# Kernel tuning notes

Hardware: AMD Instinct MI355X
Metric: run time of the kernel (lower is better)

## Reference

```python
import jax, jax.numpy as jnp
import numpy as np

# Dimensions (babyGPT-50m: GPT-2-small-ish)
B, T, V, C, H, L = 2, 1024, 50257, 768, 12, 6
D = C // H
STD = 0.02
EPS = 1e-5


def _normal(k, shape):
    return (jax.random.normal(k, shape, dtype=jnp.float32) * STD)


def setup_inputs() -> dict:
    key = jax.random.key(0)
    ks = jax.random.split(key, 12)
    inp = {
        "idx": jax.random.randint(ks[0], (B, T), 0, V, dtype=jnp.int64 if jax.config.jax_enable_x64 else jnp.int32),
        "tok_emb": _normal(ks[1], (V, C)),
        "pos_emb": _normal(ks[2], (1, T, C)),
        # per-layer params stacked along leading L axis
        "ln1_g": jnp.ones((L, C), jnp.float32),
        "ln1_b": jnp.zeros((L, C), jnp.float32),
        "Wq": _normal(ks[3], (L, C, C)), "bq": jnp.zeros((L, C), jnp.float32),
        "Wk": _normal(ks[4], (L, C, C)), "bk": jnp.zeros((L, C), jnp.float32),
        "Wv": _normal(ks[5], (L, C, C)), "bv": jnp.zeros((L, C), jnp.float32),
        "Wp": _normal(ks[6], (L, C, C)), "bp": jnp.zeros((L, C), jnp.float32),
        "ln2_g": jnp.ones((L, C), jnp.float32),
        "ln2_b": jnp.zeros((L, C), jnp.float32),
        "Wf1": _normal(ks[7], (L, C, 4 * C)), "bf1": jnp.zeros((L, 4 * C), jnp.float32),
        "Wf2": _normal(ks[8], (L, 4 * C, C)), "bf2": jnp.zeros((L, C), jnp.float32),
        "lnf_g": jnp.ones((C,), jnp.float32),
        "lnf_b": jnp.zeros((C,), jnp.float32),
        "head_W": _normal(ks[9], (C, V)),  # head has bias=False
    }
    return inp


def _ln(x, g, b):
    m = jnp.mean(x, axis=-1, keepdims=True)
    v = jnp.var(x, axis=-1, keepdims=True)
    return (x - m) * jax.lax.rsqrt(v + EPS) * g + b


def _gpt_forward(idx, tok_emb, pos_emb, ln1_g, ln1_b, Wq, bq, Wk, bk, Wv, bv,
                 Wp, bp, ln2_g, ln2_b, Wf1, bf1, Wf2, bf2, lnf_g, lnf_b, head_W):
    x = tok_emb[idx] + pos_emb[:, :T]          # [B,T,C]; dropout is identity (eval)
    causal = jnp.tril(jnp.ones((T, T), bool))  # same tril mask as the buffer
    scale = 1.0 / np.sqrt(D).astype(np.float32)

    def block(x, p):
        g1, b1, wq, bq_, wk, bk_, wv, bv_, wp, bp_, g2, b2, w1, b1f, w2, b2f = p
        h = _ln(x, g1, b1)
        q = (h @ wq + bq_).reshape(B, T, H, D)
        k = (h @ wk + bk_).reshape(B, T, H, D)
        v = (h @ wv + bv_).reshape(B, T, H, D)
        att = jnp.einsum('bthd,bshd->bhts', q, k) * scale   # [B,H,T,T]
        att = jnp.where(causal, att, jnp.float32(-10000.0))  # masked_fill value
        att = jax.nn.softmax(att, axis=-1)
        y = jnp.einsum('bhts,bshd->bthd', att, v).reshape(B, T, C)
        x = x + y @ wp + bp_
        h2 = _ln(x, g2, b2)
        ff = jax.nn.gelu(h2 @ w1 + b1f, approximate=False) @ w2 + b2f  # exact GELU, dropout=eval
        return x + ff, None

    layer_params = (ln1_g, ln1_b, Wq, bq, Wk, bk, Wv, bv, Wp, bp,
                    ln2_g, ln2_b, Wf1, bf1, Wf2, bf2)
    x, _ = jax.lax.scan(block, x, layer_params)
    x = _ln(x, lnf_g, lnf_b)
    return x @ head_W  # logits [B,T,V]


def reference(idx, tok_emb, pos_emb, ln1_g, ln1_b, Wq, bq, Wk, bk, Wv, bv,
              Wp, bp, ln2_g, ln2_b, Wf1, bf1, Wf2, bf2, lnf_g, lnf_b, head_W):
    return _gpt_forward(idx, tok_emb, pos_emb, ln1_g, ln1_b, Wq, bq, Wk, bk, Wv, bv,
                        Wp, bp, ln2_g, ln2_b, Wf1, bf1, Wf2, bf2, lnf_g, lnf_b, head_W)
```

## Files before the change

### kernel.cpp

```cpp
#include <hip/hip_runtime.h>
#include <hip/hip_bf16.h>
#include <math.h>

#define Bsz 2
#define Tt 1024
#define Vv 50257
#define Cc 768
#define Hh 12
#define Ll 6
#define NTOK (Bsz*Tt)
#define VPAD 50432

typedef __attribute__((ext_vector_type(8))) short bf16x8;
typedef __attribute__((ext_vector_type(8))) unsigned short u16x8;
typedef __attribute__((ext_vector_type(4))) unsigned short u16x4;
typedef __attribute__((ext_vector_type(4))) float f32x4;
typedef unsigned short u16;

static __device__ __forceinline__ u16 f2bf(float f){
  unsigned u = __float_as_uint(f);
  u += 0x7FFF + ((u >> 16) & 1);
  return (u16)(u >> 16);
}
static __device__ __forceinline__ float bf2f(u16 h){
  return __uint_as_float(((unsigned)h) << 16);
}

#define GL16(g,l) __builtin_amdgcn_global_load_lds( \
    (const __attribute__((address_space(1))) void*)(g), \
    (__attribute__((address_space(3))) void*)(l), 16, 0, 0)
#define WAITVM(n) asm volatile("s_waitcnt vmcnt(%0)" :: "n"(n) : "memory")

__global__ void embed_kernel(const int* __restrict__ idx, const float* __restrict__ tok,
                             const float* __restrict__ pos, float* __restrict__ x){
  const int C4 = Cc/4;
  int i = blockIdx.x * 256 + threadIdx.x;
  if (i >= NTOK*C4) return;
  int tk = i / C4, c4 = i % C4;
  int row = idx[tk];
  int t = tk % Tt;
  float4 a = ((const float4*)tok)[(size_t)row*C4 + c4];
  float4 p = ((const float4*)pos)[(size_t)t*C4 + c4];
  float4 r; r.x=a.x+p.x; r.y=a.y+p.y; r.z=a.z+p.z; r.w=a.w+p.w;
  ((float4*)x)[i] = r;
}

__global__ void ln_kernel(const float* __restrict__ in, const float* __restrict__ g,
                          const float* __restrict__ bt, u16* __restrict__ out){
  int row = blockIdx.x, tid = threadIdx.x;
  const float* r = in + (size_t)row*Cc;
  float v0=r[tid], v1=r[tid+256], v2=r[tid+512];
  float s  = v0+v1+v2;
  float s2 = v0*v0+v1*v1+v2*v2;
  #pragma unroll
  for (int off=32; off; off>>=1){ s += __shfl_xor(s,off); s2 += __shfl_xor(s2,off); }
  __shared__ float red[8];
  int wid = tid >> 6;
  if ((tid & 63) == 0){ red[wid]=s; red[4+wid]=s2; }
  __syncthreads();
  float S  = red[0]+red[1]+red[2]+red[3];
  float S2 = red[4]+red[5]+red[6]+red[7];
  float mean = S * (1.0f/Cc);
  float var  = S2 * (1.0f/Cc) - mean*mean;
  float rstd = rsqrtf(var + 1e-5f);
  u16* o = out + (size_t)row*Cc;
  o[tid]     = f2bf((v0-mean)*rstd*g[tid]     + bt[tid]);
  o[tid+256] = f2bf((v1-mean)*rstd*g[tid+256] + bt[tid+256]);
  o[tid+512] = f2bf((v2-mean)*rstd*g[tid+512] + bt[tid+512]);
}

__global__ void wtrans_kernel(const float* __restrict__ in, u16* __restrict__ out,
                              int K, int N, int Npad, size_t lsi, size_t lso){
  __shared__ float t[64][33];
  const float* inp = in + (size_t)blockIdx.z*lsi;
  u16* op = out + (size_t)blockIdx.z*lso;
  int n0 = blockIdx.x*32, k0 = blockIdx.y*64;
  int tx = threadIdx.x, ty = threadIdx.y;
  #pragma unroll
  for (int i=0;i<8;i++){
    int k = k0+ty+i*8, n = n0+tx;
    t[ty+i*8][tx] = (n < N) ? inp[(size_t)k*N + n] : 0.f;
  }
  __syncthreads();
  #pragma unroll
  for (int i=0;i<2;i++){
    int nl = i*16 + ty*2 + (tx>>4);
    int kl = (tx&15)*4;
    int n = n0 + nl;
    if (n < Npad){
      u16x4 pk;
      pk[0] = f2bf(t[kl+0][nl]); pk[1] = f2bf(t[kl+1][nl]);
      pk[2] = f2bf(t[kl+2][nl]); pk[3] = f2bf(t[kl+3][nl]);
      *(u16x4*)&op[(size_t)n*K + k0 + kl] = pk;
    }
  }
}

__global__ void vtrans_kernel(const u16* __restrict__ qkv, u16* __restrict__ vT){
  __shared__ u16 s[32][33];
  int bh = blockIdx.z; int b = bh/Hh, h = bh - b*Hh;
  int t0 = blockIdx.x*32, d0 = blockIdx.y*32;
  int tx=threadIdx.x, ty=threadIdx.y;
  #pragma unroll
  for (int i=0;i<4;i++)
    s[ty+i*8][tx] = qkv[(size_t)(b*Tt + t0+ty+i*8)*2304 + 1536 + h*64 + d0 + tx];
  __syncthreads();
  #pragma unroll
  for (int i=0;i<4;i++)
    vT[((size_t)bh*64 + d0+ty+i*8)*Tt + t0 + tx] = s[tx][ty+i*8];
}

__global__ void bconcat_kernel(const float* __restrict__ bq, const float* __restrict__ bk,
                               const float* __restrict__ bv, float* __restrict__ o){
  int i = blockIdx.x*256 + threadIdx.x;
  if (i >= Ll*2304) return;
  int l = i/2304, j = i - l*2304;
  o[i] = (j < 768) ? bq[l*768+j] : (j < 1536) ? bk[l*768+j-768] : bv[l*768+j-1536];
}

__global__ __launch_bounds__(256) void flash_kernel(
    const u16* __restrict__ qkv, const u16* __restrict__ vT, u16* __restrict__ y){
  __shared__ u16 Ks[2][64*64];
  __shared__ u16 Vs[2][64*64];
  __shared__ u16 Ps[4][16*64];
  int bx = blockIdx.x;
  int bh = blockIdx.y; int b = bh/Hh, h = bh - b*Hh;
  int q0 = bx*64;
  int tid = threadIdx.x, lane = tid&63, wid = tid>>6;
  const size_t tokbase = (size_t)b*Tt;
  int arow = lane&15, akof = (lane>>4)*8;
  bf16x8 qa[2];
  #pragma unroll
  for (int ks=0;ks<2;ks++)
    qa[ks] = *(const bf16x8*)&qkv[(tokbase + q0 + wid*16 + arow)*2304
                                  + h*64 + ks*32 + akof];
  int srow = lane>>3;
  int sbyte = ((lane&7)*16) ^ (srow<<4);
  const u16* kbase = qkv + tokbase*2304 + 768 + h*64;
  const u16* vbase = vT + (size_t)bh*64*Tt;
  auto STAGEKV = [&](int t, int bb){
    int j0 = t*64;
    #pragma unroll
    for (int c=0;c<2;c++){
      int r = wid*16 + c*8 + srow;
      GL16(kbase + (size_t)(j0 + r)*2304 + (sbyte>>1), &Ks[bb][(wid*16 + c*8)*64]);
      GL16(vbase + (size_t)r*Tt + j0 + (sbyte>>1),     &Vs[bb][(wid*16 + c*8)*64]);
    }
  };
  float m_r[4], l_r[4];
  f32x4 o_acc[4] = {};
  #pragma unroll
  for (int jj=0;jj<4;jj++){ m_r[jj] = -1e30f; l_r[jj] = 0.f; }

  int njt = bx + 1;
  STAGEKV(0, 0);
  asm volatile("s_waitcnt vmcnt(0)" ::: "memory");
  __builtin_amdgcn_s_barrier();
  for (int t=0; t<njt; t++){
    int cur = t&1;
    if (t+1 < njt) STAGEKV(t+1, cur^1);
    int j0 = t*64;
    f32x4 sacc[4] = {};
    #pragma unroll
    for (int ks=0;ks<2;ks++){
      bf16x8 kf[4];
      #pragma unroll
      for (int ni=0;ni<4;ni++){
        int s16 = ni*16 + (lane&15);
        int kb = (ks*64 + (lane>>4)*16) ^ ((s16&7)<<4);
        kf[ni] = *(const bf16x8*)((const char*)&Ks[cur][0] + s16*128 + kb);
      }
      #pragma unroll
      for (int ni=0;ni<4;ni++)
        sacc[ni] = __builtin_amdgcn_mfma_f32_16x16x32_bf16(qa[ks], kf[ni], sacc[ni], 0,0,0);
    }
    float tmax[4];
    #pragma unroll
    for (int jj=0;jj<4;jj++) tmax[jj] = -1e30f;
    #pragma unroll
    for (int ni=0;ni<4;ni++)
      #pragma unroll
      for (int jj=0;jj<4;jj++){
        float v = sacc[ni][jj]*0.125f;
        int sg = j0 + ni*16 + (lane&15);
        int tg = q0 + wid*16 + (lane>>4)*4 + jj;
        v = (sg <= tg) ? v : -1e30f;
        sacc[ni][jj] = v;
        tmax[jj] = fmaxf(tmax[jj], v);
      }
    #pragma unroll
    for (int jj=0;jj<4;jj++){
      float tm = tmax[jj];
      tm = fmaxf(tm, __shfl_xor(tm,1)); tm = fmaxf(tm, __shfl_xor(tm,2));
      tm = fmaxf(tm, __shfl_xor(tm,4)); tm = fmaxf(tm, __shfl_xor(tm,8));
      float mn = fmaxf(m_r[jj], tm);
      float al = __expf(m_r[jj] - mn);
      m_r[jj] = mn;
      l_r[jj] *= al;
      tmax[jj] = al;
    }
    float tsum[4] = {};
    #pragma unroll
    for (int ni=0;ni<4;ni++)
      #pragma unroll
      for (int jj=0;jj<4;jj++){
        float p = __expf(sacc[ni][jj] - m_r[jj]);
        tsum[jj] += p;
        int pr = (lane>>4)*4 + jj;
        int pcb = (2*(ni*16 + (lane&15))) ^ ((pr&7)<<4);
        *(u16*)((char*)&Ps[wid][0] + pr*128 + pcb) = f2bf(p);
      }
    #pragma unroll
    for (int jj=0;jj<4;jj++){
      float ts = tsum[jj];
      ts += __shfl_xor(ts,1); ts += __shfl_xor(ts,2);
      ts += __shfl_xor(ts,4); ts += __shfl_xor(ts,8);
      l_r[jj] += ts;
      float al = tmax[jj];
      #pragma unroll
      for (int ni2=0;ni2<4;ni2++) o_acc[ni2][jj] *= al;
    }
    #pragma unroll
    for (int ks2=0;ks2<2;ks2++){
      bf16x8 pa, vf[4];
      int prr = lane&15;
      int pb = (ks2*64 + (lane>>4)*16) ^ ((prr&7)<<4);
      pa = *(const bf16x8*)((const char*)&Ps[wid][0] + prr*128 + pb);
      #pragma unroll
      for (int ni2=0;ni2<4;ni2++){
        int d16 = ni2*16 + (lane&15);
        int sb = (ks2*64 + (lane>>4)*16) ^ ((d16&7)<<4);
        vf[ni2] = *(const bf16x8*)((const char*)&Vs[cur][0] + d16*128 + sb);
      }
      #pragma unroll
      for (int ni2=0;ni2<4;ni2++)
        o_acc[ni2] = __builtin_amdgcn_mfma_f32_16x16x32_bf16(pa, vf[ni2], o_acc[ni2], 0,0,0);
    }
    asm volatile("s_waitcnt vmcnt(0) lgkmcnt(0)" ::: "memory");
    __builtin_amdgcn_s_barrier();
  }
  #pragma unroll
  for (int jj=0;jj<4;jj++){
    float inv = 1.0f / l_r[jj];
    int tok2 = q0 + wid*16 + (lane>>4)*4 + jj;
    size_t rb = (tokbase + tok2)*Cc + h*64;
    #pragma unroll
    for (int ni2=0;ni2<4;ni2++)
      y[rb + ni2*16 + (lane&15)] = f2bf(o_acc[ni2][jj] * inv);
  }
}

template<int NBUF, int NTHR, int WN, int BM, int BN,
         bool BIAS, bool RESID, bool GELU, bool OUTBF, bool ROWSCAN>
__global__ __launch_bounds__(NTHR) void mm_kernel(
    const u16* __restrict__ A, const u16* __restrict__ Bm,
    const float* __restrict__ bias, const float* __restrict__ resid,
    void* __restrict__ out, int N, int K, int lda, int ldb, int ldc)
{
  constexpr int WAVES = NTHR/64;
  constexpr int WM    = WAVES/WN;
  constexpr int FM    = BM/(WM*16);
  constexpr int FN    = BN/(WN*16);
  constexpr int CPW   = FN*16;
  constexpr int ESTR  = CPW + 4;
  constexpr int ABUF  = BM*64;
  constexpr int BBUF  = BN*64;
  constexpr int ARPW  = BM/WAVES;
  constexpr int BRPW  = BN/WAVES;
  constexpr int ACALLS = ARPW/8;
  constexpr int BCALLS = BRPW/8;
  constexpr int LOADS = ACALLS + BCALLS;
  constexpr int SMEM_STAGE = NBUF*(ABUF+BBUF)*2;
  constexpr int SMEM_EPI   = WAVES*16*ESTR*4;
  constexpr int SMEMB = SMEM_STAGE > SMEM_EPI ? SMEM_STAGE : SMEM_EPI;
  __shared__ __align__(16) char smem[SMEMB];
  u16* As = (u16*)smem;
  u16* Bs = As + NBUF*ABUF;

  int bx = blockIdx.x, by = blockIdx.y;
  {
    int gx = gridDim.x;
    int nwg = gx * gridDim.y;
    int flat = by*gx + bx;
    int qq = nwg >> 3, rr = nwg & 7;
    int xcd = flat & 7, lid = flat >> 3;
    int swz = (xcd < rr) ? xcd*(qq+1) + lid : rr*(qq+1) + (xcd-rr)*qq + lid;
    bx = swz % gx; by = swz / gx;
  }
  int m0 = bx*BM, n0 = by*BN;
  int tid = threadIdx.x, lane = tid & 63, wid = tid >> 6;
  int r0 = (wid/WN)*(BM/WM), c0 = (wid%WN)*(BN/WN);
  int lrow = lane & 15;
  int sswz = ((lane & 7) ^ (lane >> 3)) * 8;
  const u16* Ap = A + (size_t)(m0 + wid*ARPW + (lane>>3))*lda + sswz;
  const u16* Bp = Bm + (size_t)(n0 + wid*BRPW + (lane>>3))*ldb + sswz;
  int cof0 = (((lane>>4)    ) ^ (lane&7)) << 4;
  int cof1 = (((lane>>4) + 4) ^ (lane&7)) << 4;
  int nt = K/64;
  auto STAGE = [&](int t, int bb){
    int kk = t*64;
    u16* Al = As + bb*ABUF + (wid*ARPW)*64;
    #pragma unroll
    for (int c=0;c<ACALLS;c++)
      GL16(Ap + kk + (size_t)(c*8)*lda, Al + c*512);
    u16* Bl = Bs + bb*BBUF + (wid*BRPW)*64;
    #pragma unroll
    for (int c=0;c<BCALLS;c++)
      GL16(Bp + kk + (size_t)(c*8)*ldb, Bl + c*512);
  };
  f32x4 acc[FM][FN] = {};
  if constexpr (NBUF==2){
    STAGE(0, 0);
    WAITVM(0);
    __builtin_amdgcn_s_barrier();
  } else {
    STAGE(0, 0);
    if (nt > 1) STAGE(1, 1);
    WAITVM(LOADS);
    __builtin_amdgcn_s_barrier();
  }
  for (int t = 0; t < nt; t++){
    int bb = (NBUF==2) ? (t & 1) : (t % 3);
    if constexpr (NBUF==2){
      if (t+1 < nt) STAGE(t+1, (t+1)&1);
    } else {
      if (t+2 < nt) STAGE(t+2, (t+2)%3);
    }
    const char* Ab2 = (const char*)(As + bb*ABUF);
    const char* Bb2 = (const char*)(Bs + bb*BBUF);
    #pragma unroll
    for (int ks=0;ks<2;ks++){
      int cof = ks ? cof1 : cof0;
      bf16x8 af[FM], bfr[FN];
      #pragma unroll
      for (int m=0;m<FM;m++) af[m] = *(const bf16x8*)(Ab2 + (r0 + m*16 + lrow)*128 + cof);
      #pragma unroll
      for (int n=0;n<FN;n++) bfr[n] = *(const bf16x8*)(Bb2 + (c0 + n*16 + lrow)*128 + cof);
      #pragma unroll
      for (int m=0;m<FM;m++)
        #pragma unroll
        for (int n=0;n<FN;n++)
          acc[m][n] = __builtin_amdgcn_mfma_f32_16x16x32_bf16(af[m], bfr[n], acc[m][n], 0,0,0);
    }
    if constexpr (NBUF==2){
      asm volatile("s_waitcnt vmcnt(0) lgkmcnt(0)" ::: "memory");
    } else {
      if (t+2 < nt) WAITVM(LOADS); else WAITVM(0);
    }
    __builtin_amdgcn_s_barrier();
  }

  float* ebuf = (float*)smem + wid*16*ESTR;
  int er = lane >> 2;
  int ec = (lane & 3) * (CPW/4);
  #pragma unroll
  for (int m=0;m<FM;m++){
    #pragma unroll
    for (int n=0;n<FN;n++)
      #pragma unroll
      for (int j=0;j<4;j++)
        ebuf[((lane>>4)*4+j)*ESTR + n*16 + (lane&15)] = acc[m][n][j];
    __builtin_amdgcn_s_waitcnt(0);
    if constexpr (ROWSCAN){
      #pragma unroll
      for (int rr2=0; rr2<16; rr2++){
        int gr2 = m0 + r0 + m*16 + rr2;
        int gc2 = n0 + c0 + lane;
        float v = ebuf[rr2*ESTR + lane];
        if (gc2 < N)
          __builtin_nontemporal_store(v, &((float*)out)[(size_t)gr2*ldc + gc2]);
      }
    } else {
      int grow = m0 + r0 + m*16 + er;
      int gcol = n0 + c0 + ec;
      size_t rbase = (size_t)grow*ldc;
      if constexpr (OUTBF){
        u16 tmp[CPW/4];
        #pragma unroll
        for (int q=0;q<FN;q++){
          float4 v = *(const float4*)&ebuf[er*ESTR + ec + q*4];
          float f0=v.x, f1=v.y, f2=v.z, f3=v.w;
          if (BIAS){
            float4 b4 = *(const float4*)&bias[gcol + q*4];
            f0+=b4.x; f1+=b4.y; f2+=b4.z; f3+=b4.w;
          }
          if (GELU){
            f0 = 0.5f*f0*(1.f+erff(f0*0.70710678118654752f));
            f1 = 0.5f*f1*(1.f+erff(f1*0.70710678118654752f));
            f2 = 0.5f*f2*(1.f+erff(f2*0.70710678118654752f));
            f3 = 0.5f*f3*(1.f+erff(f3*0.70710678118654752f));
          }
          tmp[q*4+0]=f2bf(f0); tmp[q*4+1]=f2bf(f1);
          tmp[q*4+2]=f2bf(f2); tmp[q*4+3]=f2bf(f3);
        }
        #pragma unroll
        for (int s2=0; s2<CPW/32; s2++)
          *(u16x8*)&((u16*)out)[rbase + gcol + s2*8] = *(const u16x8*)&tmp[s2*8];
      } else {
        #pragma unroll
        for (int q=0;q<FN;q++){
          float4 v = *(const float4*)&ebuf[er*ESTR + ec + q*4];
          float f0=v.x, f1=v.y, f2=v.z, f3=v.w;
          if (BIAS){
            float4 b4 = *(const float4*)&bias[gcol + q*4];
            f0+=b4.x; f1+=b4.y; f2+=b4.z; f3+=b4.w;
          }
          if (GELU){
            f0 = 0.5f*f0*(1.f+erff(f0*0.70710678118654752f));
            f1 = 0.5f*f1*(1.f+erff(f1*0.70710678118654752f));
            f2 = 0.5f*f2*(1.f+erff(f2*0.70710678118654752f));
            f3 = 0.5f*f3*(1.f+erff(f3*0.70710678118654752f));
          }
          if (RESID){
            float4 r4 = *(const float4*)&resid[rbase + gcol + q*4];
            f0+=r4.x; f1+=r4.y; f2+=r4.z; f3+=r4.w;
          }
          float4 o4; o4.x=f0; o4.y=f1; o4.z=f2; o4.w=f3;
          *(float4*)&((float*)out)[rbase + gcol + q*4] = o4;
        }
      }
    }
  }
}

extern "C" void kernel_launch(void* const* d_in, const int* in_sizes, int n_in,
                              void* d_out, int out_size, void* d_ws, size_t ws_size,
                              hipStream_t stream){
  const int*   idx  = (const int*)d_in[0];
  const float* tok  = (const float*)d_in[1];
  const float* pos  = (const float*)d_in[2];
  const float* ln1g = (const float*)d_in[3];
  const float* ln1b = (const float*)d_in[4];
  const float* Wq   = (const float*)d_in[5];
  const float* bq   = (const float*)d_in[6];
  const float* Wk   = (const float*)d_in[7];
  const float* bk   = (const float*)d_in[8];
  const float* Wv   = (const float*)d_in[9];
  const float* bv   = (const float*)d_in[10];
  const float* Wp   = (const float*)d_in[11];
  const float* bp   = (const float*)d_in[12];
  const float* ln2g = (const float*)d_in[13];
  const float* ln2b = (const float*)d_in[14];
  const float* Wf1  = (const float*)d_in[15];
  const float* bf1  = (const float*)d_in[16];
  const float* Wf2  = (const float*)d_in[17];
  const float* bf2  = (const float*)d_in[18];
  const float* lnfg = (const float*)d_in[19];
  const float* lnfb = (const float*)d_in[20];
  const float* headW= (const float*)d_in[21];
  float* outp = (float*)d_out;

  char* w = (char*)d_ws;
  u16* wqkvT = (u16*)w;  w += (size_t)Ll*2304*768*2;
  u16* wpT   = (u16*)w;  w += (size_t)Ll*768*768*2;
  u16* wf1T  = (u16*)w;  w += (size_t)Ll*3072*768*2;
  u16* wf2T  = (u16*)w;  w += (size_t)Ll*768*3072*2;
  u16* headT = (u16*)w;  w += (size_t)VPAD*768*2;
  float* bqkv= (float*)w;w += (size_t)Ll*2304*4;
  float* x   = (float*)w;w += (size_t)NTOK*Cc*4;
  u16* h     = (u16*)w;  w += (size_t)NTOK*Cc*2;
  u16* qkv   = (u16*)w;  w += (size_t)NTOK*2304*2;
  u16* vT    = (u16*)w;  w += (size_t)Bsz*Hh*64*Tt*2;
  u16* y     = (u16*)w;  w += (size_t)NTOK*Cc*2;
  u16* ff    = (u16*)w;  w += (size_t)NTOK*4*Cc*2;

  dim3 tb(32,8);
  wtrans_kernel<<<dim3(24,12,Ll), tb, 0, stream>>>(Wq, wqkvT,          768, 768, 768, (size_t)Cc*Cc, (size_t)2304*768);
  wtrans_kernel<<<dim3(24,12,Ll), tb, 0, stream>>>(Wk, wqkvT+768*768,  768, 768, 768, (size_t)Cc*Cc, (size_t)2304*768);
  wtrans_kernel<<<dim3(24,12,Ll), tb, 0, stream>>>(Wv, wqkvT+1536*768, 768, 768, 768, (size_t)Cc*Cc, (size_t)2304*768);
  wtrans_kernel<<<dim3(24,12,Ll), tb, 0, stream>>>(Wp, wpT,            768, 768, 768, (size_t)Cc*Cc, (size_t)768*768);
  wtrans_kernel<<<dim3(96,12,Ll), tb, 0, stream>>>(Wf1, wf1T,          768, 3072, 3072, (size_t)Cc*4*Cc, (size_t)3072*768);
  wtrans_kernel<<<dim3(24,48,Ll), tb, 0, stream>>>(Wf2, wf2T,          3072, 768, 768, (size_t)4*Cc*Cc, (size_t)768*3072);
  wtrans_kernel<<<dim3(VPAD/32,12,1), tb, 0, stream>>>(headW, headT, 768, Vv, VPAD, 0, 0);
  bconcat_kernel<<<(Ll*2304+255)/256, 256, 0, stream>>>(bq, bk, bv, bqkv);

  embed_kernel<<<NTOK*(Cc/4)/256, 256, 0, stream>>>(idx, tok, pos, x);

  for (int l=0;l<Ll;l++){
    ln_kernel<<<NTOK, 256, 0, stream>>>(x, ln1g+l*Cc, ln1b+l*Cc, h);
    mm_kernel<2,256,2,64,128,true,false,false,true,false><<<dim3(32,18,1), 256, 0, stream>>>(
        h, wqkvT+(size_t)l*2304*768, bqkv+l*2304, nullptr, qkv, 2304, 768, 768, 768, 2304);
    vtrans_kernel<<<dim3(32,2,Bsz*Hh), tb, 0, stream>>>(qkv, vT);
    flash_kernel<<<dim3(Tt/64, Bsz*Hh), 256, 0, stream>>>(qkv, vT, y);
    mm_kernel<3,256,2,64,64,true,true,false,false,false><<<dim3(32,12,1), 256, 0, stream>>>(
        y, wpT+(size_t)l*768*768, bp+l*Cc, x, x, 768, 768, 768, 768, 768);
    ln_kernel<<<NTOK, 256, 0, stream>>>(x, ln2g+l*Cc, ln2b+l*Cc, h);
    mm_kernel<2,256,2,64,128,true,false,true,true,false><<<dim3(32,24,1), 256, 0, stream>>>(
        h, wf1T+(size_t)l*3072*768, bf1+(size_t)l*4*Cc, nullptr, ff, 3072, 768, 768, 768, 3072);
    mm_kernel<3,256,2,64,64,true,true,false,false,false><<<dim3(32,12,1), 256, 0, stream>>>(
        ff, wf2T+(size_t)l*768*3072, bf2+l*Cc, x, x, 768, 3072, 3072, 3072, 768);
  }
  ln_kernel<<<NTOK, 256, 0, stream>>>(x, lnfg, lnfb, h);
  mm_kernel<3,512,4,128,256,false,false,false,false,true><<<dim3(16,VPAD/256,1), 512, 0, stream>>>(
      h, headT, nullptr, nullptr, outp, Vv, 768, 768, 768, Vv);
}
```

Measured before the change: 1.150 ms.

## Add BK=32 GEMM path, retile LM head, vectorize weight transpose

The GEMM kernel gains a BK template parameter, with a new 32-wide K-tile path that uses its own LDS swizzle and row mapping. The LM head GEMM switches from 512-thread 128x256 triple-buffered tiles to 256-thread 128x128 double-buffered tiles with BK=32. The vocabulary padding drops from 50432 to 50304 to cut wasted columns. The weight transpose kernel now reads float4 rows, converts to bf16 before staging in LDS, and writes 16-byte stores, lowering setup traffic. The new swizzle path carries a risk of bank conflicts or indexing errors.

```diff
diff --git a/kernel.cpp b/kernel.cpp
--- a/kernel.cpp
+++ b/kernel.cpp
@@ -9,7 +9,7 @@
 #define Hh 12
 #define Ll 6
 #define NTOK (Bsz*Tt)
-#define VPAD 50432
+#define VPAD 50304
 
 typedef __attribute__((ext_vector_type(8))) short bf16x8;
 typedef __attribute__((ext_vector_type(8))) unsigned short u16x8;
@@ -71,28 +71,38 @@
 
 __global__ void wtrans_kernel(const float* __restrict__ in, u16* __restrict__ out,
                               int K, int N, int Npad, size_t lsi, size_t lso){
-  __shared__ float t[64][33];
+  __shared__ u16 t[64][68];
   const float* inp = in + (size_t)blockIdx.z*lsi;
   u16* op = out + (size_t)blockIdx.z*lso;
-  int n0 = blockIdx.x*32, k0 = blockIdx.y*64;
-  int tx = threadIdx.x, ty = threadIdx.y;
-  #pragma unroll
-  for (int i=0;i<8;i++){
-    int k = k0+ty+i*8, n = n0+tx;
-    t[ty+i*8][tx] = (n < N) ? inp[(size_t)k*N + n] : 0.f;
+  int n0 = blockIdx.x*64, k0 = blockIdx.y*64;
+  int tid = threadIdx.x;
+  #pragma unroll
+  for (int i=0;i<4;i++){
+    int e = tid + 256*i;
+    int k = e >> 4, n4 = (e & 15) * 4;
+    int n = n0 + n4;
+    const float* rowp = inp + (size_t)(k0+k)*N;
+    float4 v;
+    if (n + 3 < N) v = *(const float4*)&rowp[n];
+    else {
+      v.x = (n   < N) ? rowp[n  ] : 0.f;
+      v.y = (n+1 < N) ? rowp[n+1] : 0.f;
+      v.z = (n+2 < N) ? rowp[n+2] : 0.f;
+      v.w = (n+3 < N) ? rowp[n+3] : 0.f;
+    }
+    u16x4 pk; pk[0]=f2bf(v.x); pk[1]=f2bf(v.y); pk[2]=f2bf(v.z); pk[3]=f2bf(v.w);
+    *(u16x4*)&t[k][n4] = pk;
   }
   __syncthreads();
   #pragma unroll
   for (int i=0;i<2;i++){
-    int nl = i*16 + ty*2 + (tx>>4);
-    int kl = (tx&15)*4;
-    int n = n0 + nl;
-    if (n < Npad){
-      u16x4 pk;
-      pk[0] = f2bf(t[kl+0][nl]); pk[1] = f2bf(t[kl+1][nl]);
-      pk[2] = f2bf(t[kl+2][nl]); pk[3] = f2bf(t[kl+3][nl]);
-      *(u16x4*)&op[(size_t)n*K + k0 + kl] = pk;
-    }
+    int e = tid + 256*i;
+    int n = e >> 3, k8 = (e & 7) * 8;
+    u16x8 pk;
+    #pragma unroll
+    for (int q=0;q<8;q++) pk[q] = t[k8+q][n];
+    if (n0 + n < Npad)
+      *(u16x8*)&op[(size_t)(n0+n)*K + k0 + k8] = pk;
   }
 }
 
@@ -250,7 +260,7 @@
   }
 }
 
-template<int NBUF, int NTHR, int WN, int BM, int BN,
+template<int NBUF, int NTHR, int WN, int BM, int BN, int BK,
          bool BIAS, bool RESID, bool GELU, bool OUTBF, bool ROWSCAN>
 __global__ __launch_bounds__(NTHR) void mm_kernel(
     const u16* __restrict__ A, const u16* __restrict__ Bm,
@@ -261,14 +271,16 @@
   constexpr int WM    = WAVES/WN;
   constexpr int FM    = BM/(WM*16);
   constexpr int FN    = BN/(WN*16);
+  constexpr int KSTEPS = BK/32;
   constexpr int CPW   = FN*16;
   constexpr int ESTR  = CPW + 4;
-  constexpr int ABUF  = BM*64;
-  constexpr int BBUF  = BN*64;
+  constexpr int ABUF  = BM*BK;
+  constexpr int BBUF  = BN*BK;
   constexpr int ARPW  = BM/WAVES;
   constexpr int BRPW  = BN/WAVES;
-  constexpr int ACALLS = ARPW/8;
-  constexpr int BCALLS = BRPW/8;
+  constexpr int RPC   = (BK==64) ? 8 : 16;
+  constexpr int ACALLS = ARPW/RPC;
+  constexpr int BCALLS = BRPW/RPC;
   constexpr int LOADS = ACALLS + BCALLS;
   constexpr int SMEM_STAGE = NBUF*(ABUF+BBUF)*2;
   constexpr int SMEM_EPI   = WAVES*16*ESTR*4;
@@ -291,22 +303,22 @@
   int tid = threadIdx.x, lane = tid & 63, wid = tid >> 6;
   int r0 = (wid/WN)*(BM/WM), c0 = (wid%WN)*(BN/WN);
   int lrow = lane & 15;
-  int sswz = ((lane & 7) ^ (lane >> 3)) * 8;
-  const u16* Ap = A + (size_t)(m0 + wid*ARPW + (lane>>3))*lda + sswz;
-  const u16* Bp = Bm + (size_t)(n0 + wid*BRPW + (lane>>3))*ldb + sswz;
-  int cof0 = (((lane>>4)    ) ^ (lane&7)) << 4;
-  int cof1 = (((lane>>4) + 4) ^ (lane&7)) << 4;
-  int nt = K/64;
+  int rl, sswz;
+  if constexpr (BK==64){ rl = lane>>3; sswz = ((lane&7) ^ (lane>>3)) * 8; }
+  else                 { rl = lane>>2; sswz = ((lane&3) ^ ((lane>>3)&3)) * 8; }
+  const u16* Ap = A + (size_t)(m0 + wid*ARPW + rl)*lda + sswz;
+  const u16* Bp = Bm + (size_t)(n0 + wid*BRPW + rl)*ldb + sswz;
+  int nt = K/BK;
   auto STAGE = [&](int t, int bb){
-    int kk = t*64;
-    u16* Al = As + bb*ABUF + (wid*ARPW)*64;
+    int kk = t*BK;
+    u16* Al = As + bb*ABUF + (wid*ARPW)*BK;
     #pragma unroll
     for (int c=0;c<ACALLS;c++)
-      GL16(Ap + kk + (size_t)(c*8)*lda, Al + c*512);
-    u16* Bl = Bs + bb*BBUF + (wid*BRPW)*64;
+      GL16(Ap + kk + (size_t)(c*RPC)*lda, Al + c*512);
+    u16* Bl = Bs + bb*BBUF + (wid*BRPW)*BK;
     #pragma unroll
     for (int c=0;c<BCALLS;c++)
-      GL16(Bp + kk + (size_t)(c*8)*ldb, Bl + c*512);
+      GL16(Bp + kk + (size_t)(c*RPC)*ldb, Bl + c*512);
   };
   f32x4 acc[FM][FN] = {};
   if constexpr (NBUF==2){
@@ -329,13 +341,15 @@
     const char* Ab2 = (const char*)(As + bb*ABUF);
     const char* Bb2 = (const char*)(Bs + bb*BBUF);
     #pragma unroll
-    for (int ks=0;ks<2;ks++){
-      int cof = ks ? cof1 : cof0;
+    for (int ks=0;ks<KSTEPS;ks++){
+      int cof;
+      if constexpr (BK==64) cof = ((ks*4 + (lane>>4)) ^ (lane&7)) << 4;
+      else                  cof = ((lane>>4) ^ (((lane&15)>>1)&3)) << 4;
       bf16x8 af[FM], bfr[FN];
       #pragma unroll
-      for (int m=0;m<FM;m++) af[m] = *(const bf16x8*)(Ab2 + (r0 + m*16 + lrow)*128 + cof);
-      #pragma unroll
-      for (int n=0;n<FN;n++) bfr[n] = *(const bf16x8*)(Bb2 + (c0 + n*16 + lrow)*128 + cof);
+      for (int m=0;m<FM;m++) af[m] = *(const bf16x8*)(Ab2 + (r0 + m*16 + lrow)*(BK*2) + cof);
+      #pragma unroll
+      for (int n=0;n<FN;n++) bfr[n] = *(const bf16x8*)(Bb2 + (c0 + n*16 + lrow)*(BK*2) + cof);
       #pragma unroll
       for (int m=0;m<FM;m++)
         #pragma unroll
@@ -465,32 +479,32 @@
   u16* ff    = (u16*)w;  w += (size_t)NTOK*4*Cc*2;
 
   dim3 tb(32,8);
-  wtrans_kernel<<<dim3(24,12,Ll), tb, 0, stream>>>(Wq, wqkvT,          768, 768, 768, (size_t)Cc*Cc, (size_t)2304*768);
-  wtrans_kernel<<<dim3(24,12,Ll), tb, 0, stream>>>(Wk, wqkvT+768*768,  768, 768, 768, (size_t)Cc*Cc, (size_t)2304*768);
-  wtrans_kernel<<<dim3(24,12,Ll), tb, 0, stream>>>(Wv, wqkvT+1536*768, 768, 768, 768, (size_t)Cc*Cc, (size_t)2304*768);
-  wtrans_kernel<<<dim3(24,12,Ll), tb, 0, stream>>>(Wp, wpT,            768, 768, 768, (size_t)Cc*Cc, (size_t)768*768);
-  wtrans_kernel<<<dim3(96,12,Ll), tb, 0, stream>>>(Wf1, wf1T,          768, 3072, 3072, (size_t)Cc*4*Cc, (size_t)3072*768);
-  wtrans_kernel<<<dim3(24,48,Ll), tb, 0, stream>>>(Wf2, wf2T,          3072, 768, 768, (size_t)4*Cc*Cc, (size_t)768*3072);
-  wtrans_kernel<<<dim3(VPAD/32,12,1), tb, 0, stream>>>(headW, headT, 768, Vv, VPAD, 0, 0);
+  wtrans_kernel<<<dim3(12,12,Ll), 256, 0, stream>>>(Wq, wqkvT,          768, 768, 768, (size_t)Cc*Cc, (size_t)2304*768);
+  wtrans_kernel<<<dim3(12,12,Ll), 256, 0, stream>>>(Wk, wqkvT+768*768,  768, 768, 768, (size_t)Cc*Cc, (size_t)2304*768);
+  wtrans_kernel<<<dim3(12,12,Ll), 256, 0, stream>>>(Wv, wqkvT+1536*768, 768, 768, 768, (size_t)Cc*Cc, (size_t)2304*768);
+  wtrans_kernel<<<dim3(12,12,Ll), 256, 0, stream>>>(Wp, wpT,            768, 768, 768, (size_t)Cc*Cc, (size_t)768*768);
+  wtrans_kernel<<<dim3(48,12,Ll), 256, 0, stream>>>(Wf1, wf1T,          768, 3072, 3072, (size_t)Cc*4*Cc, (size_t)3072*768);
+  wtrans_kernel<<<dim3(12,48,Ll), 256, 0, stream>>>(Wf2, wf2T,          3072, 768, 768, (size_t)4*Cc*Cc, (size_t)768*3072);
+  wtrans_kernel<<<dim3(VPAD/64,12,1), 256, 0, stream>>>(headW, headT, 768, Vv, VPAD, 0, 0);
   bconcat_kernel<<<(Ll*2304+255)/256, 256, 0, stream>>>(bq, bk, bv, bqkv);
 
   embed_kernel<<<NTOK*(Cc/4)/256, 256, 0, stream>>>(idx, tok, pos, x);
 
   for (int l=0;l<Ll;l++){
     ln_kernel<<<NTOK, 256, 0, stream>>>(x, ln1g+l*Cc, ln1b+l*Cc, h);
-    mm_kernel<2,256,2,64,128,true,false,false,true,false><<<dim3(32,18,1), 256, 0, stream>>>(
+    mm_kernel<2,256,2,64,128,64,true,false,false,true,false><<<dim3(32,18,1), 256, 0, stream>>>(
         h, wqkvT+(size_t)l*2304*768, bqkv+l*2304, nullptr, qkv, 2304, 768, 768, 768, 2304);
     vtrans_kernel<<<dim3(32,2,Bsz*Hh), tb, 0, stream>>>(qkv, vT);
     flash_kernel<<<dim3(Tt/64, Bsz*Hh), 256, 0, stream>>>(qkv, vT, y);
-    mm_kernel<3,256,2,64,64,true,true,false,false,false><<<dim3(32,12,1), 256, 0, stream>>>(
+    mm_kernel<3,256,2,64,64,64,true,true,false,false,false><<<dim3(32,12,1), 256, 0, stream>>>(
         y, wpT+(size_t)l*768*768, bp+l*Cc, x, x, 768, 768, 768, 768, 768);
     ln_kernel<<<NTOK, 256, 0, stream>>>(x, ln2g+l*Cc, ln2b+l*Cc, h);
-    mm_kernel<2,256,2,64,128,true,false,true,true,false><<<dim3(32,24,1), 256, 0, stream>>>(
+    mm_kernel<2,256,2,64,128,64,true,false,true,true,false><<<dim3(32,24,1), 256, 0, stream>>>(
         h, wf1T+(size_t)l*3072*768, bf1+(size_t)l*4*Cc, nullptr, ff, 3072, 768, 768, 768, 3072);
-    mm_kernel<3,256,2,64,64,true,true,false,false,false><<<dim3(32,12,1), 256, 0, stream>>>(
+    mm_kernel<3,256,2,64,64,64,true,true,false,false,false><<<dim3(32,12,1), 256, 0, stream>>>(
         ff, wf2T+(size_t)l*768*3072, bf2+l*Cc, x, x, 768, 3072, 3072, 3072, 768);
   }
   ln_kernel<<<NTOK, 256, 0, stream>>>(x, lnfg, lnfb, h);
-  mm_kernel<3,512,4,128,256,false,false,false,false,true><<<dim3(16,VPAD/256,1), 512, 0, stream>>>(
+  mm_kernel<2,256,2,128,128,32,false,false,false,false,true><<<dim3(16,VPAD/128,1), 256, 0, stream>>>(
       h, headT, nullptr, nullptr, outp, Vv, 768, 768, 768, Vv);
 }
```

Result: faster. 1.097 ms (-4.6%).
